# Kernel tuning notes

Measured on AMD Instinct MI355X. Metric: run time of the kernel, lower is better.

Reference implementation:

```python
import jax, jax.numpy as jnp
import numpy as np

N = 50000      # num nodes
E = 800000     # num edges (avg degree 16)
D = 128        # in_dim


def setup_inputs() -> dict:
    key = jax.random.key(0)
    k1, k2, k3, k4, k5, k6 = jax.random.split(key, 6)
    h = jax.random.normal(k1, (N, D), dtype=jnp.float32)
    deg = jax.random.uniform(k2, (N,), dtype=jnp.float32)  # degree-norm scalars d
    # xavier_normal_ with gain=1.414 on Linear(2D, 1)
    std = 1.414 * np.sqrt(2.0 / (2 * D + 1))
    gate_w = jax.random.normal(k3, (1, 2 * D), dtype=jnp.float32) * std
    gate_b = jax.random.normal(k4, (1,), dtype=jnp.float32) * 0.01
    src = jax.random.randint(k5, (E,), 0, N, dtype=jnp.int64)
    dst = jax.random.randint(k6, (E,), 0, N, dtype=jnp.int64)
    return {"h": h, "deg": deg, "gate_w": gate_w, "gate_b": gate_b,
            "src": src, "dst": dst}


def reference(h, deg, gate_w, gate_b, src, dst):
    # Split gate weight so we never materialize the [E, 2D] concat:
    # gate(cat([h_dst, h_src])) == h_dst @ w_d.T + h_src @ w_s.T + b
    d_feat = h.shape[1]
    w_d = gate_w[:, :d_feat]   # [1, D] applied to dst features
    w_s = gate_w[:, d_feat:]   # [1, D] applied to src features
    hs = h[src]                # [E, D] gather of source node features
    hd = h[dst]                # [E, D] gather of dest node features
    a = jnp.tanh(hd @ w_d.T + hs @ w_s.T + gate_b).squeeze(-1)  # [E]
    e = a * deg[dst] * deg[src]                                  # [E] (dropout = identity, eval)
    # message = h[src] * e ; aggregate sum at dst
    z = jax.ops.segment_sum(hs * e[:, None], dst, num_segments=h.shape[0])  # [N, D]
    return z
```

## Files before the change

### kernel.cpp

```cpp
#include <hip/hip_runtime.h>

#define N_NODES 50000
#define N_EDGES 800000
#define DFEAT   128
#define CAP     48
#define NBINS   256
#define NPB     196
#define BINCAP  3700
#define CHUNK   4096

__device__ __forceinline__ unsigned bf16_rne(float f) {
    unsigned u = __float_as_uint(f);
    return (u + 0x7FFFu + ((u >> 16) & 1u)) >> 16;
}

__global__ __launch_bounds__(256) void k1_dots(const float* __restrict__ h,
                                               const float* __restrict__ gate_w,
                                               const float* __restrict__ deg,
                                               float4* __restrict__ nodetab,
                                               int* __restrict__ counts,
                                               unsigned* __restrict__ hb) {
    int node = (blockIdx.x * 256 + threadIdx.x) >> 6;
    int lane = threadIdx.x & 63;
    if (node >= N_NODES) return;
    const float2* h2 = (const float2*)(h + (size_t)node * DFEAT);
    float2 hv = h2[lane];
    if (hb) {
        unsigned lo = bf16_rne(hv.x);
        unsigned hi = bf16_rne(hv.y);
        hb[(size_t)node * 64 + lane] = lo | (hi << 16);
    }
    float2 wd = ((const float2*)gate_w)[lane];
    float2 ws = ((const float2*)(gate_w + DFEAT))[lane];
    float vd = hv.x * wd.x + hv.y * wd.y;
    float vs = hv.x * ws.x + hv.y * ws.y;
    #pragma unroll
    for (int off = 32; off > 0; off >>= 1) {
        vd += __shfl_down(vd, off, 64);
        vs += __shfl_down(vs, off, 64);
    }
    if (lane == 0) {
        nodetab[node] = make_float4(vd, vs, deg[node], 0.0f);
        counts[node] = 0;
    }
}

__global__ __launch_bounds__(256) void k2a_bin(const int* __restrict__ src,
                                               const int* __restrict__ dst,
                                               const float4* __restrict__ nodetab,
                                               const float* __restrict__ gate_b,
                                               int* __restrict__ gbin_cnt,
                                               uint2* __restrict__ binned) {
    __shared__ uint2 stage[CHUNK];
    __shared__ int bcnt[NBINS], bcur[NBINS], gbase[NBINS];
    int tid = threadIdx.x;
    for (int i = tid; i < NBINS; i += 256) { bcnt[i] = 0; bcur[i] = 0; }
    __syncthreads();

    int e0 = blockIdx.x * CHUNK;
    float bb = gate_b[0];
    for (int i = tid; i < CHUNK; i += 256) {
        int e = e0 + i;
        unsigned m = 0xFFFFFFFFu; float w = 0.f;
        if (e < N_EDGES) {
            int s = src[e], d = dst[e];
            float4 ns = nodetab[s];
            float4 nd = nodetab[d];
            float a = tanhf(nd.x + ns.y + bb);
            w = a * nd.z * ns.z;
            int bin  = d / NPB;
            int dlow = d - bin * NPB;
            m = (unsigned)s | ((unsigned)dlow << 16) | ((unsigned)bin << 24);
            atomicAdd(&bcnt[bin], 1);
        }
        stage[i] = make_uint2(m, __float_as_uint(w));
    }
    __syncthreads();
    for (int i = tid; i < NBINS; i += 256)
        if (bcnt[i] > 0) gbase[i] = atomicAdd(&gbin_cnt[i], bcnt[i]);
    __syncthreads();
    for (int i = tid; i < CHUNK; i += 256) {
        uint2 r = stage[i];
        if (r.x != 0xFFFFFFFFu) {
            int bin = r.x >> 24;
            int pos = atomicAdd(&bcur[bin], 1);
            int idx = gbase[bin] + pos;
            if (idx < BINCAP)
                binned[(size_t)bin * BINCAP + idx] = r;
        }
    }
}

__global__ __launch_bounds__(256) void k2b_bucket(const uint2* __restrict__ binned,
                                                  const int* __restrict__ gbin_cnt,
                                                  uint2* __restrict__ bucket,
                                                  int* __restrict__ counts) {
    __shared__ int  lcnt[NPB];
    __shared__ uint2 lbuck[NPB * CAP];
    int tid = threadIdx.x, bin = blockIdx.x;
    for (int i = tid; i < NPB; i += 256) lcnt[i] = 0;
    __syncthreads();

    int cnt = gbin_cnt[bin]; if (cnt > BINCAP) cnt = BINCAP;
    const uint2* bsrc = binned + (size_t)bin * BINCAP;
    for (int i = tid; i < cnt; i += 256) {
        uint2 r = bsrc[i];
        int dlow = (r.x >> 16) & 0xFF;
        int pos = atomicAdd(&lcnt[dlow], 1);
        if (pos < CAP) lbuck[dlow * CAP + pos] = make_uint2(r.x & 0xFFFFu, r.y);
    }
    __syncthreads();

    int nbase = bin * NPB;
    int nvalid = N_NODES - nbase; if (nvalid > NPB) nvalid = NPB;
    for (int i = tid; i < nvalid; i += 256) {
        int c = lcnt[i];
        counts[nbase + i] = (c > CAP) ? CAP : c;
    }
    int limit = nvalid * CAP;
    uint2* dstp = bucket + (size_t)nbase * CAP;
    for (int i = tid; i < limit; i += 256) dstp[i] = lbuck[i];
}

__global__ __launch_bounds__(256) void k2_edge(const int* __restrict__ src,
                                               const int* __restrict__ dst,
                                               const float4* __restrict__ nodetab,
                                               const float* __restrict__ gate_b,
                                               int* __restrict__ counts,
                                               int2* __restrict__ bucket) {
    int e = blockIdx.x * 256 + threadIdx.x;
    if (e >= N_EDGES) return;
    int s = src[e], d = dst[e];
    float4 ns = nodetab[s];
    float4 nd = nodetab[d];
    float a = tanhf(nd.x + ns.y + gate_b[0]);
    float w = a * nd.z * ns.z;
    int pos = atomicAdd(&counts[d], 1);
    if (pos < CAP)
        bucket[(size_t)d * CAP + pos] = make_int2(s, __float_as_int(w));
}

__device__ __forceinline__ void bf4_fma(float4& a, float w, uint2 q) {
    a.x += w * __uint_as_float(q.x << 16);
    a.y += w * __uint_as_float(q.x & 0xFFFF0000u);
    a.z += w * __uint_as_float(q.y << 16);
    a.w += w * __uint_as_float(q.y & 0xFFFF0000u);
}

__global__ __launch_bounds__(256) void k5_gather_bf16(const int2* __restrict__ bucket,
                                                      const int* __restrict__ counts,
                                                      const unsigned* __restrict__ hb,
                                                      float* __restrict__ z) {
    int node = (blockIdx.x * 256 + threadIdx.x) >> 6;
    int lane = threadIdx.x & 63;
    if (node >= N_NODES) return;
    int half = lane >> 5;
    int fl   = lane & 31;
    int cnt = counts[node];
    if (cnt > CAP) cnt = CAP;
    const int2* b = bucket + (size_t)node * CAP;
    const uint2* hb2 = (const uint2*)hb;

    float4 a0 = make_float4(0.f,0.f,0.f,0.f);
    float4 a1 = make_float4(0.f,0.f,0.f,0.f);
    float4 a2 = make_float4(0.f,0.f,0.f,0.f);
    float4 a3 = make_float4(0.f,0.f,0.f,0.f);

    int p = 0;
    for (; p + 8 <= cnt; p += 8) {
        int2 e0 = b[p     + half];
        int2 e1 = b[p + 2 + half];
        int2 e2 = b[p + 4 + half];
        int2 e3 = b[p + 6 + half];
        uint2 q0 = hb2[(size_t)e0.x * 32 + fl];
        uint2 q1 = hb2[(size_t)e1.x * 32 + fl];
        uint2 q2 = hb2[(size_t)e2.x * 32 + fl];
        uint2 q3 = hb2[(size_t)e3.x * 32 + fl];
        bf4_fma(a0, __int_as_float(e0.y), q0);
        bf4_fma(a1, __int_as_float(e1.y), q1);
        bf4_fma(a2, __int_as_float(e2.y), q2);
        bf4_fma(a3, __int_as_float(e3.y), q3);
    }
    for (; p < cnt; p += 2) {
        int q = p + half;
        if (q < cnt) {
            int2 e = b[q];
            uint2 qv = hb2[(size_t)e.x * 32 + fl];
            bf4_fma(a0, __int_as_float(e.y), qv);
        }
    }

    a0.x += a1.x + a2.x + a3.x;
    a0.y += a1.y + a2.y + a3.y;
    a0.z += a1.z + a2.z + a3.z;
    a0.w += a1.w + a2.w + a3.w;

    float ox = __shfl_down(a0.x, 32, 64);
    float oy = __shfl_down(a0.y, 32, 64);
    float oz = __shfl_down(a0.z, 32, 64);
    float ow = __shfl_down(a0.w, 32, 64);
    if (half == 0) {
        a0.x += ox; a0.y += oy; a0.z += oz; a0.w += ow;
        ((float4*)z)[(size_t)node * 32 + fl] = a0;
    }
}

__global__ __launch_bounds__(256) void k5_gather_f32(const int2* __restrict__ bucket,
                                                     const int* __restrict__ counts,
                                                     const float* __restrict__ h,
                                                     float* __restrict__ z) {
    int node = (blockIdx.x * 256 + threadIdx.x) >> 6;
    int lane = threadIdx.x & 63;
    if (node >= N_NODES) return;
    int half = lane >> 5;
    int fl   = lane & 31;
    int cnt = counts[node];
    if (cnt > CAP) cnt = CAP;
    const int2* b = bucket + (size_t)node * CAP;
    const float4* h4 = (const float4*)h;

    float4 a0 = make_float4(0.f,0.f,0.f,0.f);
    float4 a1 = make_float4(0.f,0.f,0.f,0.f);

    int p = 0;
    for (; p + 4 <= cnt; p += 4) {
        int2 e0 = b[p     + half];
        int2 e1 = b[p + 2 + half];
        float4 h0 = h4[(size_t)e0.x * 32 + fl];
        float4 h1 = h4[(size_t)e1.x * 32 + fl];
        float w0 = __int_as_float(e0.y);
        float w1 = __int_as_float(e1.y);
        a0.x += w0*h0.x; a0.y += w0*h0.y; a0.z += w0*h0.z; a0.w += w0*h0.w;
        a1.x += w1*h1.x; a1.y += w1*h1.y; a1.z += w1*h1.z; a1.w += w1*h1.w;
    }
    for (; p < cnt; p += 2) {
        int q = p + half;
        if (q < cnt) {
            int2 e = b[q];
            float4 hv = h4[(size_t)e.x * 32 + fl];
            float w = __int_as_float(e.y);
            a0.x += w*hv.x; a0.y += w*hv.y; a0.z += w*hv.z; a0.w += w*hv.w;
        }
    }
    a0.x += a1.x; a0.y += a1.y; a0.z += a1.z; a0.w += a1.w;

    float ox = __shfl_down(a0.x, 32, 64);
    float oy = __shfl_down(a0.y, 32, 64);
    float oz = __shfl_down(a0.z, 32, 64);
    float ow = __shfl_down(a0.w, 32, 64);
    if (half == 0) {
        a0.x += ox; a0.y += oy; a0.z += oz; a0.w += ow;
        ((float4*)z)[(size_t)node * 32 + fl] = a0;
    }
}

extern "C" void kernel_launch(void* const* d_in, const int* in_sizes, int n_in,
                              void* d_out, int out_size, void* d_ws, size_t ws_size,
                              hipStream_t stream) {
    const float* h      = (const float*)d_in[0];
    const float* deg    = (const float*)d_in[1];
    const float* gate_w = (const float*)d_in[2];
    const float* gate_b = (const float*)d_in[3];
    const int*   src    = (const int*)d_in[4];
    const int*   dst    = (const int*)d_in[5];
    float* z = (float*)d_out;

    float4*   nodetab = (float4*)d_ws;
    int*      counts  = (int*)(nodetab + N_NODES);
    uint2*    bucket  = (uint2*)(counts + N_NODES);
    unsigned* hb      = (unsigned*)(bucket + (size_t)N_NODES * CAP);
    int*      gbin    = (int*)(hb + (size_t)N_NODES * 64);
    uint2*    binned  = (uint2*)(gbin + NBINS);
    const size_t NEED_BF16 = 800000u + 200000u + 19200000u + 12800000u;
    const size_t NEED_BIN  = NEED_BF16 + 1024u + (size_t)NBINS * BINCAP * 8u;
    bool use_bf16 = (ws_size >= NEED_BF16);
    bool use_bin  = (ws_size >= NEED_BIN);

    int nodeBlocks = (N_NODES * 64 + 255) / 256;
    int edgeBlocks = (N_EDGES + 255) / 256;
    int binBlocks  = (N_EDGES + CHUNK - 1) / CHUNK;

    k1_dots<<<nodeBlocks, 256, 0, stream>>>(h, gate_w, deg, nodetab, counts,
                                            use_bf16 ? hb : nullptr);
    if (use_bin) {
        hipMemsetAsync(gbin, 0, NBINS * sizeof(int), stream);
        k2a_bin<<<binBlocks, 256, 0, stream>>>(src, dst, nodetab, gate_b, gbin, binned);
        k2b_bucket<<<NBINS, 256, 0, stream>>>(binned, gbin, bucket, counts);
    } else {
        k2_edge<<<edgeBlocks, 256, 0, stream>>>(src, dst, nodetab, gate_b,
                                                counts, (int2*)bucket);
    }
    if (use_bf16)
        k5_gather_bf16<<<nodeBlocks, 256, 0, stream>>>((const int2*)bucket, counts, hb, z);
    else
        k5_gather_f32<<<nodeBlocks, 256, 0, stream>>>((const int2*)bucket, counts, h, z);
}
```

Before: 161.4 us.

## Pack bucket entries into 32-bit (16-bit src + bf16 weight), fuse bin-count reset

Each bucket entry now holds a 16-bit source index and a bf16 edge weight in one 32-bit word instead of an int2. This halves bucket write and read traffic and shared memory in k2b_bucket. The gather loop now takes 16 entries per iteration with clamped indices and zeroed weights, so there is no scalar tail loop. The separate memset of the bin counters moves into block 0 of k1_dots. The risks are lower weight precision and a silent limit to sources below 65536, while N is 50000; in k2_edge a source index above 65535 would overlap the weight bits.

```diff
diff --git a/kernel.cpp b/kernel.cpp
--- a/kernel.cpp
+++ b/kernel.cpp
@@ -19,7 +19,11 @@
                                                const float* __restrict__ deg,
                                                float4* __restrict__ nodetab,
                                                int* __restrict__ counts,
-                                               unsigned* __restrict__ hb) {
+                                               unsigned* __restrict__ hb,
+                                               int* __restrict__ gbin) {
+    if (gbin && blockIdx.x == 0) {
+        for (int i = threadIdx.x; i < NBINS; i += 256) gbin[i] = 0;
+    }
     int node = (blockIdx.x * 256 + threadIdx.x) >> 6;
     int lane = threadIdx.x & 63;
     if (node >= N_NODES) return;
@@ -93,10 +97,10 @@
 
 __global__ __launch_bounds__(256) void k2b_bucket(const uint2* __restrict__ binned,
                                                   const int* __restrict__ gbin_cnt,
-                                                  uint2* __restrict__ bucket,
+                                                  unsigned* __restrict__ bucket,
                                                   int* __restrict__ counts) {
-    __shared__ int  lcnt[NPB];
-    __shared__ uint2 lbuck[NPB * CAP];
+    __shared__ int lcnt[NPB];
+    __shared__ unsigned lbuck[NPB * CAP];
     int tid = threadIdx.x, bin = blockIdx.x;
     for (int i = tid; i < NPB; i += 256) lcnt[i] = 0;
     __syncthreads();
@@ -106,8 +110,9 @@
     for (int i = tid; i < cnt; i += 256) {
         uint2 r = bsrc[i];
         int dlow = (r.x >> 16) & 0xFF;
+        unsigned packed = (r.x & 0xFFFFu) | (bf16_rne(__uint_as_float(r.y)) << 16);
         int pos = atomicAdd(&lcnt[dlow], 1);
-        if (pos < CAP) lbuck[dlow * CAP + pos] = make_uint2(r.x & 0xFFFFu, r.y);
+        if (pos < CAP) lbuck[dlow * CAP + pos] = packed;
     }
     __syncthreads();
 
@@ -118,7 +123,7 @@
         counts[nbase + i] = (c > CAP) ? CAP : c;
     }
     int limit = nvalid * CAP;
-    uint2* dstp = bucket + (size_t)nbase * CAP;
+    unsigned* dstp = bucket + (size_t)nbase * CAP;
     for (int i = tid; i < limit; i += 256) dstp[i] = lbuck[i];
 }
 
@@ -127,7 +132,7 @@
                                                const float4* __restrict__ nodetab,
                                                const float* __restrict__ gate_b,
                                                int* __restrict__ counts,
-                                               int2* __restrict__ bucket) {
+                                               unsigned* __restrict__ bucket) {
     int e = blockIdx.x * 256 + threadIdx.x;
     if (e >= N_EDGES) return;
     int s = src[e], d = dst[e];
@@ -137,7 +142,7 @@
     float w = a * nd.z * ns.z;
     int pos = atomicAdd(&counts[d], 1);
     if (pos < CAP)
-        bucket[(size_t)d * CAP + pos] = make_int2(s, __float_as_int(w));
+        bucket[(size_t)d * CAP + pos] = (unsigned)s | (bf16_rne(w) << 16);
 }
 
 __device__ __forceinline__ void bf4_fma(float4& a, float w, uint2 q) {
@@ -147,7 +152,7 @@
     a.w += w * __uint_as_float(q.y & 0xFFFF0000u);
 }
 
-__global__ __launch_bounds__(256) void k5_gather_bf16(const int2* __restrict__ bucket,
+__global__ __launch_bounds__(256) void k5_gather_bf16(const unsigned* __restrict__ bucket,
                                                       const int* __restrict__ counts,
                                                       const unsigned* __restrict__ hb,
                                                       float* __restrict__ z) {
@@ -158,7 +163,7 @@
     int fl   = lane & 31;
     int cnt = counts[node];
     if (cnt > CAP) cnt = CAP;
-    const int2* b = bucket + (size_t)node * CAP;
+    const unsigned* b = bucket + (size_t)node * CAP;
     const uint2* hb2 = (const uint2*)hb;
 
     float4 a0 = make_float4(0.f,0.f,0.f,0.f);
@@ -166,28 +171,43 @@
     float4 a2 = make_float4(0.f,0.f,0.f,0.f);
     float4 a3 = make_float4(0.f,0.f,0.f,0.f);
 
-    int p = 0;
-    for (; p + 8 <= cnt; p += 8) {
-        int2 e0 = b[p     + half];
-        int2 e1 = b[p + 2 + half];
-        int2 e2 = b[p + 4 + half];
-        int2 e3 = b[p + 6 + half];
-        uint2 q0 = hb2[(size_t)e0.x * 32 + fl];
-        uint2 q1 = hb2[(size_t)e1.x * 32 + fl];
-        uint2 q2 = hb2[(size_t)e2.x * 32 + fl];
-        uint2 q3 = hb2[(size_t)e3.x * 32 + fl];
-        bf4_fma(a0, __int_as_float(e0.y), q0);
-        bf4_fma(a1, __int_as_float(e1.y), q1);
-        bf4_fma(a2, __int_as_float(e2.y), q2);
-        bf4_fma(a3, __int_as_float(e3.y), q3);
-    }
-    for (; p < cnt; p += 2) {
-        int q = p + half;
-        if (q < cnt) {
-            int2 e = b[q];
-            uint2 qv = hb2[(size_t)e.x * 32 + fl];
-            bf4_fma(a0, __int_as_float(e.y), qv);
-        }
+    int last = cnt - 1;
+    for (int p = 0; p < cnt; p += 16) {
+        int base = p + half;
+        int i0 = base;      if (i0 > last) i0 = last;
+        int i1 = base + 2;  if (i1 > last) i1 = last;
+        int i2 = base + 4;  if (i2 > last) i2 = last;
+        int i3 = base + 6;  if (i3 > last) i3 = last;
+        int i4 = base + 8;  if (i4 > last) i4 = last;
+        int i5 = base + 10; if (i5 > last) i5 = last;
+        int i6 = base + 12; if (i6 > last) i6 = last;
+        int i7 = base + 14; if (i7 > last) i7 = last;
+        unsigned e0 = b[i0], e1 = b[i1], e2 = b[i2], e3 = b[i3];
+        unsigned e4 = b[i4], e5 = b[i5], e6 = b[i6], e7 = b[i7];
+        uint2 q0 = hb2[(size_t)(e0 & 0xFFFFu) * 32 + fl];
+        uint2 q1 = hb2[(size_t)(e1 & 0xFFFFu) * 32 + fl];
+        uint2 q2 = hb2[(size_t)(e2 & 0xFFFFu) * 32 + fl];
+        uint2 q3 = hb2[(size_t)(e3 & 0xFFFFu) * 32 + fl];
+        uint2 q4 = hb2[(size_t)(e4 & 0xFFFFu) * 32 + fl];
+        uint2 q5 = hb2[(size_t)(e5 & 0xFFFFu) * 32 + fl];
+        uint2 q6 = hb2[(size_t)(e6 & 0xFFFFu) * 32 + fl];
+        uint2 q7 = hb2[(size_t)(e7 & 0xFFFFu) * 32 + fl];
+        float w0 = (base      <= last) ? __uint_as_float(e0 & 0xFFFF0000u) : 0.f;
+        float w1 = (base + 2  <= last) ? __uint_as_float(e1 & 0xFFFF0000u) : 0.f;
+        float w2 = (base + 4  <= last) ? __uint_as_float(e2 & 0xFFFF0000u) : 0.f;
+        float w3 = (base + 6  <= last) ? __uint_as_float(e3 & 0xFFFF0000u) : 0.f;
+        float w4 = (base + 8  <= last) ? __uint_as_float(e4 & 0xFFFF0000u) : 0.f;
+        float w5 = (base + 10 <= last) ? __uint_as_float(e5 & 0xFFFF0000u) : 0.f;
+        float w6 = (base + 12 <= last) ? __uint_as_float(e6 & 0xFFFF0000u) : 0.f;
+        float w7 = (base + 14 <= last) ? __uint_as_float(e7 & 0xFFFF0000u) : 0.f;
+        bf4_fma(a0, w0, q0);
+        bf4_fma(a1, w1, q1);
+        bf4_fma(a2, w2, q2);
+        bf4_fma(a3, w3, q3);
+        bf4_fma(a0, w4, q4);
+        bf4_fma(a1, w5, q5);
+        bf4_fma(a2, w6, q6);
+        bf4_fma(a3, w7, q7);
     }
 
     a0.x += a1.x + a2.x + a3.x;
@@ -205,7 +225,7 @@
     }
 }
 
-__global__ __launch_bounds__(256) void k5_gather_f32(const int2* __restrict__ bucket,
+__global__ __launch_bounds__(256) void k5_gather_f32(const unsigned* __restrict__ bucket,
                                                      const int* __restrict__ counts,
                                                      const float* __restrict__ h,
                                                      float* __restrict__ z) {
@@ -216,7 +236,7 @@
     int fl   = lane & 31;
     int cnt = counts[node];
     if (cnt > CAP) cnt = CAP;
-    const int2* b = bucket + (size_t)node * CAP;
+    const unsigned* b = bucket + (size_t)node * CAP;
     const float4* h4 = (const float4*)h;
 
     float4 a0 = make_float4(0.f,0.f,0.f,0.f);
@@ -224,21 +244,21 @@
 
     int p = 0;
     for (; p + 4 <= cnt; p += 4) {
-        int2 e0 = b[p     + half];
-        int2 e1 = b[p + 2 + half];
-        float4 h0 = h4[(size_t)e0.x * 32 + fl];
-        float4 h1 = h4[(size_t)e1.x * 32 + fl];
-        float w0 = __int_as_float(e0.y);
-        float w1 = __int_as_float(e1.y);
+        unsigned e0 = b[p     + half];
+        unsigned e1 = b[p + 2 + half];
+        float4 h0 = h4[(size_t)(e0 & 0xFFFFu) * 32 + fl];
+        float4 h1 = h4[(size_t)(e1 & 0xFFFFu) * 32 + fl];
+        float w0 = __uint_as_float(e0 & 0xFFFF0000u);
+        float w1 = __uint_as_float(e1 & 0xFFFF0000u);
         a0.x += w0*h0.x; a0.y += w0*h0.y; a0.z += w0*h0.z; a0.w += w0*h0.w;
         a1.x += w1*h1.x; a1.y += w1*h1.y; a1.z += w1*h1.z; a1.w += w1*h1.w;
     }
     for (; p < cnt; p += 2) {
         int q = p + half;
         if (q < cnt) {
-            int2 e = b[q];
-            float4 hv = h4[(size_t)e.x * 32 + fl];
-            float w = __int_as_float(e.y);
+            unsigned e = b[q];
+            float4 hv = h4[(size_t)(e & 0xFFFFu) * 32 + fl];
+            float w = __uint_as_float(e & 0xFFFF0000u);
             a0.x += w*hv.x; a0.y += w*hv.y; a0.z += w*hv.z; a0.w += w*hv.w;
         }
     }
@@ -267,11 +287,11 @@
 
     float4*   nodetab = (float4*)d_ws;
     int*      counts  = (int*)(nodetab + N_NODES);
-    uint2*    bucket  = (uint2*)(counts + N_NODES);
+    unsigned* bucket  = (unsigned*)(counts + N_NODES);
     unsigned* hb      = (unsigned*)(bucket + (size_t)N_NODES * CAP);
     int*      gbin    = (int*)(hb + (size_t)N_NODES * 64);
     uint2*    binned  = (uint2*)(gbin + NBINS);
-    const size_t NEED_BF16 = 800000u + 200000u + 19200000u + 12800000u;
+    const size_t NEED_BF16 = 800000u + 200000u + 9600000u + 12800000u;
     const size_t NEED_BIN  = NEED_BF16 + 1024u + (size_t)NBINS * BINCAP * 8u;
     bool use_bf16 = (ws_size >= NEED_BF16);
     bool use_bin  = (ws_size >= NEED_BIN);
@@ -281,17 +301,17 @@
     int binBlocks  = (N_EDGES + CHUNK - 1) / CHUNK;
 
     k1_dots<<<nodeBlocks, 256, 0, stream>>>(h, gate_w, deg, nodetab, counts,
-                                            use_bf16 ? hb : nullptr);
+                                            use_bf16 ? hb : nullptr,
+                                            use_bin ? gbin : nullptr);
     if (use_bin) {
-        hipMemsetAsync(gbin, 0, NBINS * sizeof(int), stream);
         k2a_bin<<<binBlocks, 256, 0, stream>>>(src, dst, nodetab, gate_b, gbin, binned);
         k2b_bucket<<<NBINS, 256, 0, stream>>>(binned, gbin, bucket, counts);
     } else {
         k2_edge<<<edgeBlocks, 256, 0, stream>>>(src, dst, nodetab, gate_b,
-                                                counts, (int2*)bucket);
+                                                counts, bucket);
     }
     if (use_bf16)
-        k5_gather_bf16<<<nodeBlocks, 256, 0, stream>>>((const int2*)bucket, counts, hb, z);
+        k5_gather_bf16<<<nodeBlocks, 256, 0, stream>>>(bucket, counts, hb, z);
     else
-        k5_gather_f32<<<nodeBlocks, 256, 0, stream>>>((const int2*)bucket, counts, h, z);
-}
+        k5_gather_f32<<<nodeBlocks, 256, 0, stream>>>(bucket, counts, h, z);
+}
```

Measured after the change: 157.8 us. 2.2% less time.
